# Performance work log

Hardware: AMD Instinct MI355X
Metric: run time of the kernel (lower is better)

Reference implementation:

```python
import jax, jax.numpy as jnp
import numpy as np

B, L = 8, 2048          # images, lines per image
C_IN, HW = 256, 128     # backbone feature channels, spatial size
DIM_LOI = 128
N_PTS0, N_PTS1 = 32, 8  # sampled points per line, after maxpool
SCALE = N_PTS0 // N_PTS1
EPS = 1e-5


def setup_inputs() -> dict:
    key = jax.random.key(0)
    ks = jax.random.split(key, 24)
    d = {}
    d['feature'] = jax.random.normal(ks[0], (B, C_IN, HW, HW), jnp.float32)
    # line endpoints in pixel coords [0, 128)
    d['lines'] = jax.random.uniform(ks[1], (B, L, 2, 2), jnp.float32) * HW
    # fc1: 1x1 conv 256 -> 128
    d['fc1_w'] = jax.random.normal(ks[2], (DIM_LOI, C_IN), jnp.float32) * 0.05
    d['fc1_b'] = jnp.zeros((DIM_LOI,), jnp.float32)
    planes = DIM_LOI // 2
    def bn(k, c):
        k1, k2, k3 = jax.random.split(k, 3)
        return (jax.random.normal(k1, (c,), jnp.float32) * 0.1 + 1.0,
                jax.random.normal(k2, (c,), jnp.float32) * 0.1,
                jax.random.normal(k3, (c,), jnp.float32) * 0.05,
                jax.random.uniform(jax.random.fold_in(k, 7), (c,), jnp.float32, 0.5, 1.5))
    d['bn1_g'], d['bn1_b'], d['bn1_m'], d['bn1_v'] = bn(ks[3], DIM_LOI)
    d['conv1_w'] = jax.random.normal(ks[4], (planes, DIM_LOI), jnp.float32) * 0.05
    d['conv1_b'] = jnp.zeros((planes,), jnp.float32)
    d['bn2_g'], d['bn2_b'], d['bn2_m'], d['bn2_v'] = bn(ks[5], planes)
    d['conv2_w'] = jax.random.normal(ks[6], (planes, planes, 3), jnp.float32) * 0.05
    d['conv2_b'] = jnp.zeros((planes,), jnp.float32)
    d['bn3_g'], d['bn3_b'], d['bn3_m'], d['bn3_v'] = bn(ks[7], planes)
    d['conv3_w'] = jax.random.normal(ks[8], (DIM_LOI, planes), jnp.float32) * 0.05
    d['conv3_b'] = jnp.zeros((DIM_LOI,), jnp.float32)
    d['fc2_w'] = jax.random.normal(ks[9], (1, DIM_LOI * N_PTS1), jnp.float32) * 0.02
    d['fc2_b'] = jnp.zeros((1,), jnp.float32)
    return d


def _bn(x, g, b, m, v):
    # x: [N, C, T], eval-mode batchnorm
    s = g * jax.lax.rsqrt(v + EPS)
    return x * s[None, :, None] + (b - m * s)[None, :, None]


def _loi_forward(feature, lines, fc1_w, fc1_b,
                 bn1_g, bn1_b, bn1_m, bn1_v, conv1_w, conv1_b,
                 bn2_g, bn2_b, bn2_m, bn2_v, conv2_w, conv2_b,
                 bn3_g, bn3_b, bn3_m, bn3_v, conv3_w, conv3_b,
                 fc2_w, fc2_b):
    # fc1: 1x1 conv -> [B, DIM_LOI, H, W]
    x = jnp.einsum('oc,bchw->bohw', fc1_w, feature) + fc1_b[None, :, None, None]

    # sample N_PTS0 points per line: p = p0*lam + p1*(1-lam) - 0.5
    lam = jnp.linspace(0.0, 1.0, N_PTS0, dtype=lines.dtype)  # [P]
    pts = (lines[:, :, 0, None, :] * lam[None, None, :, None]
           + lines[:, :, 1, None, :] * (1.0 - lam[None, None, :, None]) - 0.5)  # [B,L,P,2]
    px, py = pts[..., 0], pts[..., 1]
    px0 = jnp.clip(jnp.floor(px), 0.0, HW - 1.0)
    py0 = jnp.clip(jnp.floor(py), 0.0, HW - 1.0)
    px1 = jnp.clip(px0 + 1.0, 0.0, HW - 1.0)
    py1 = jnp.clip(py0 + 1.0, 0.0, HW - 1.0)
    px0l, py0l = px0.astype(jnp.int32), py0.astype(jnp.int32)
    px1l, py1l = px1.astype(jnp.int32), py1.astype(jnp.int32)

    def gather(f, ix, iy):  # f: [C,H,W], ix/iy: [L,P] -> [C,L,P]
        return f[:, ix, iy]

    gat = jax.vmap(gather)  # over batch
    xp = (gat(x, px0l, py0l) * ((px1 - px) * (py1 - py))[:, None]
          + gat(x, px1l, py0l) * ((px - px0) * (py1 - py))[:, None]
          + gat(x, px0l, py1l) * ((px1 - px) * (py - py0))[:, None]
          + gat(x, px1l, py1l) * ((px - px0) * (py - py0))[:, None])  # [B,C,L,P]

    xp = xp.transpose(0, 2, 1, 3).reshape(B * L, DIM_LOI, N_PTS0)  # [N,C,P]
    # MaxPool1d(kernel=stride=SCALE)
    xp = xp.reshape(B * L, DIM_LOI, N_PTS1, SCALE).max(axis=-1)  # [N,C,T=8]

    # Bottleneck1D residual: x + op(x)
    h = jax.nn.relu(_bn(xp, bn1_g, bn1_b, bn1_m, bn1_v))
    h = jnp.einsum('oc,nct->not', conv1_w, h) + conv1_b[None, :, None]
    h = jax.nn.relu(_bn(h, bn2_g, bn2_b, bn2_m, bn2_v))
    h = jax.lax.conv_general_dilated(h, conv2_w, (1,), [(1, 1)],
                                     dimension_numbers=('NCH', 'OIH', 'NCH'))
    h = h + conv2_b[None, :, None]
    h = jax.nn.relu(_bn(h, bn3_g, bn3_b, bn3_m, bn3_v))
    h = jnp.einsum('oc,nct->not', conv3_w, h) + conv3_b[None, :, None]
    xp = xp + h

    # fc2: ReLU -> Linear(dim_loi*n_pts1, 1)
    flat = jax.nn.relu(xp).reshape(B * L, DIM_LOI * N_PTS1)
    logits = (flat @ fc2_w.T + fc2_b).reshape(-1)  # [B*L]
    return logits


def reference(feature, lines, fc1_w, fc1_b,
              bn1_g, bn1_b, bn1_m, bn1_v, conv1_w, conv1_b,
              bn2_g, bn2_b, bn2_m, bn2_v, conv2_w, conv2_b,
              bn3_g, bn3_b, bn3_m, bn3_v, conv3_w, conv3_b,
              fc2_w, fc2_b):
    return _loi_forward(feature, lines, fc1_w, fc1_b,
                        bn1_g, bn1_b, bn1_m, bn1_v, conv1_w, conv1_b,
                        bn2_g, bn2_b, bn2_m, bn2_v, conv2_w, conv2_b,
                        bn3_g, bn3_b, bn3_m, bn3_v, conv3_w, conv3_b,
                        fc2_w, fc2_b)
```

## Files before the change

kernel.cpp:

```cpp
#include <hip/hip_runtime.h>

#define EPSBN 1e-5f

typedef _Float16 f16;
typedef _Float16 f16x8 __attribute__((ext_vector_type(8)));
typedef _Float16 f16x4 __attribute__((ext_vector_type(4)));
typedef _Float16 f16x2 __attribute__((ext_vector_type(2)));
typedef float    f32x4 __attribute__((ext_vector_type(4)));

__device__ inline unsigned int pack2(float a, float b) {
    union { f16x2 h; unsigned int u; } cv;
    cv.h[0] = (f16)a; cv.h[1] = (f16)b;
    return cv.u;
}
__device__ inline f16x4 hmax4(f16x4 a, f16x4 b) {
    f16x4 r;
    #pragma unroll
    for (int i = 0; i < 4; ++i) r[i] = a[i] > b[i] ? a[i] : b[i];
    return r;
}
__device__ inline f16x8 relu8(f16x8 v) {
    f16x8 r;
    #pragma unroll
    for (int i = 0; i < 8; ++i) r[i] = v[i] > (f16)0.f ? v[i] : (f16)0.f;
    return r;
}

__global__ void wprep_kernel(const float* __restrict__ fc1w,
                             const float* __restrict__ w1,
                             const float* __restrict__ w2,
                             const float* __restrict__ w3,
                             f16* __restrict__ dst) {
    const int i = blockIdx.x * 256 + threadIdx.x;
    float v;
    if (i < 32768)      v = fc1w[i];
    else if (i < 40960) v = w1[i - 32768];
    else if (i < 53248) {
        const int j = i - 40960, tau = j >> 12, rest = j & 4095;
        v = w2[rest * 3 + tau];
    } else              v = w3[i - 53248];
    dst[i] = (f16)v;
}

__global__ __launch_bounds__(256)
void fc1_mfma(const float* __restrict__ feat,
              const f16*   __restrict__ w16,
              const float* __restrict__ bias,
              f16*         __restrict__ xmap) {
    __shared__ f16 lds[64][136];

    const int tid  = threadIdx.x;
    const int wv   = tid >> 6, lane = tid & 63;
    const int n16  = lane & 15, quad = lane >> 4;
    const int b    = blockIdx.x & 7;
    const int p0   = (blockIdx.x >> 3) * 64;
    const int cp   = tid & 31;
    const int pg   = tid >> 5;

    f32x4 acc[8];
    #pragma unroll
    for (int nt = 0; nt < 8; ++nt) acc[nt] = (f32x4){0.f, 0.f, 0.f, 0.f};

    const float* fbase = feat + (((size_t)b) << 22) + p0 + pg * 8;
    unsigned int* ldsu = (unsigned int*)&lds[0][0];
    const int wrow = pg * 8;

    float4 c0a, c0b, c1a, c1b;
    {
        const float* r0 = fbase + (size_t)(2 * cp) * 16384;
        c0a = *(const float4*)(r0);          c0b = *(const float4*)(r0 + 4);
        c1a = *(const float4*)(r0 + 16384);  c1b = *(const float4*)(r0 + 16388);
        ldsu[(wrow + 0) * 68 + cp] = pack2(c0a.x, c1a.x);
        ldsu[(wrow + 1) * 68 + cp] = pack2(c0a.y, c1a.y);
        ldsu[(wrow + 2) * 68 + cp] = pack2(c0a.z, c1a.z);
        ldsu[(wrow + 3) * 68 + cp] = pack2(c0a.w, c1a.w);
        ldsu[(wrow + 4) * 68 + cp] = pack2(c0b.x, c1b.x);
        ldsu[(wrow + 5) * 68 + cp] = pack2(c0b.y, c1b.y);
        ldsu[(wrow + 6) * 68 + cp] = pack2(c0b.z, c1b.z);
        ldsu[(wrow + 7) * 68 + cp] = pack2(c0b.w, c1b.w);
    }

    for (int kc = 0; kc < 4; ++kc) {
        __syncthreads();
        if (kc < 3) {
            const float* r0 = fbase + (size_t)((kc + 1) * 64 + 2 * cp) * 16384;
            c0a = *(const float4*)(r0);          c0b = *(const float4*)(r0 + 4);
            c1a = *(const float4*)(r0 + 16384);  c1b = *(const float4*)(r0 + 16388);
        }
        #pragma unroll
        for (int ks = 0; ks < 2; ++ks) {
            const f16x8 a = *(const f16x8*)&lds[wv * 16 + n16][ks * 32 + quad * 8];
            #pragma unroll
            for (int nt = 0; nt < 8; ++nt) {
                const f16x8 bf = *(const f16x8*)&w16[(size_t)(nt * 16 + n16) * 256
                                                     + kc * 64 + ks * 32 + quad * 8];
                acc[nt] = __builtin_amdgcn_mfma_f32_16x16x32_f16(a, bf, acc[nt], 0, 0, 0);
            }
        }
        __syncthreads();
        if (kc < 3) {
            ldsu[(wrow + 0) * 68 + cp] = pack2(c0a.x, c1a.x);
            ldsu[(wrow + 1) * 68 + cp] = pack2(c0a.y, c1a.y);
            ldsu[(wrow + 2) * 68 + cp] = pack2(c0a.z, c1a.z);
            ldsu[(wrow + 3) * 68 + cp] = pack2(c0a.w, c1a.w);
            ldsu[(wrow + 4) * 68 + cp] = pack2(c0b.x, c1b.x);
            ldsu[(wrow + 5) * 68 + cp] = pack2(c0b.y, c1b.y);
            ldsu[(wrow + 6) * 68 + cp] = pack2(c0b.z, c1b.z);
            ldsu[(wrow + 7) * 68 + cp] = pack2(c0b.w, c1b.w);
        }
    }

    #pragma unroll
    for (int nt = 0; nt < 8; ++nt) {
        const int o = nt * 16 + n16;
        const float bo = bias[o];
        #pragma unroll
        for (int r = 0; r < 4; ++r)
            lds[wv * 16 + quad * 4 + r][o] = (f16)(acc[nt][r] + bo);
    }
    __syncthreads();

    #pragma unroll
    for (int it = 0; it < 4; ++it) {
        const int u = tid + 256 * it;
        const int row = u >> 4, cg = u & 15;
        const float4 v = *(const float4*)&lds[row][cg * 8];
        *(float4*)&xmap[(((size_t)((b << 14) + p0 + row)) << 7) + cg * 8] = v;
    }
}

__global__ __launch_bounds__(256)
void loi_kernel(const f16*   __restrict__ x,
                const float* __restrict__ lines,
                const f16*   __restrict__ wsp,
                const float* __restrict__ bn1g, const float* __restrict__ bn1b,
                const float* __restrict__ bn1m, const float* __restrict__ bn1v,
                const float* __restrict__ b1,
                const float* __restrict__ bn2g, const float* __restrict__ bn2b,
                const float* __restrict__ bn2m, const float* __restrict__ bn2v,
                const float* __restrict__ b2,
                const float* __restrict__ bn3g, const float* __restrict__ bn3b,
                const float* __restrict__ bn3m, const float* __restrict__ bn3v,
                const float* __restrict__ b3,
                const float* __restrict__ fc2w, const float* __restrict__ fc2b,
                float* __restrict__ out) {
    __shared__ f16 xp[64][136];
    __shared__ alignas(16) union {
        struct { int toff[256][4]; f16 twgt[256][4]; } tp;
        struct { f16 h1[80][72]; f16 h2[64][72]; } cv;
    } u;
    __shared__ f16 s1h[128], t1h[128];
    __shared__ float s2f[64], t2f[64], s3f[64], t3f[64], b1f[64], b2f[64];
    __shared__ float b3f[128];
    __shared__ float wsum[4][8];

    const f16* w1f16 = wsp + 32768;
    const f16* w2f16 = wsp + 40960;
    const f16* w3f16 = wsp + 53248;

    const int tid  = threadIdx.x;
    const int wv   = tid >> 6, lane = tid & 63;
    const int n16  = lane & 15, quad = lane >> 4;
    const int img  = blockIdx.x & 7;
    const int mblk = blockIdx.x >> 3;

    if (tid < 128) {
        const float s = bn1g[tid] * rsqrtf(bn1v[tid] + EPSBN);
        s1h[tid] = (f16)s; t1h[tid] = (f16)(bn1b[tid] - bn1m[tid] * s);
    }
    if (tid < 64) {
        const float s = bn2g[tid] * rsqrtf(bn2v[tid] + EPSBN);
        s2f[tid] = s; t2f[tid] = bn2b[tid] - bn2m[tid] * s;
        b1f[tid] = b1[tid];
    } else if (tid < 128) {
        const int c = tid - 64;
        const float s = bn3g[c] * rsqrtf(bn3v[c] + EPSBN);
        s3f[c] = s; t3f[c] = bn3b[c] - bn3m[c] * s;
        b2f[c] = b2[c];
    } else {
        b3f[tid - 128] = b3[tid - 128];
    }

    {
        const int li = tid >> 5, pt = tid & 31;
        const int gl = img * 2048 + mblk * 8 + li;
        const float4 ln = *(const float4*)&lines[gl * 4];
        const float lam = (float)pt * (1.0f / 31.0f);
        const float px = ln.x * lam + ln.z * (1.f - lam) - 0.5f;
        const float py = ln.y * lam + ln.w * (1.f - lam) - 0.5f;
        const float px0 = fminf(fmaxf(floorf(px), 0.f), 127.f);
        const float py0 = fminf(fmaxf(floorf(py), 0.f), 127.f);
        const float px1 = fminf(px0 + 1.f, 127.f);
        const float py1 = fminf(py0 + 1.f, 127.f);
        const int ix0 = (int)px0, iy0 = (int)py0;
        const int ix1 = (int)px1, iy1 = (int)py1;
        u.tp.toff[tid][0] = (((ix0 << 7) + iy0) << 7);
        u.tp.toff[tid][1] = (((ix1 << 7) + iy0) << 7);
        u.tp.toff[tid][2] = (((ix0 << 7) + iy1) << 7);
        u.tp.toff[tid][3] = (((ix1 << 7) + iy1) << 7);
        const float wx1 = px1 - px, wx0 = px - px0;
        const float wy1 = py1 - py, wy0 = py - py0;
        u.tp.twgt[tid][0] = (f16)(wx1 * wy1); u.tp.twgt[tid][1] = (f16)(wx0 * wy1);
        u.tp.twgt[tid][2] = (f16)(wx1 * wy0); u.tp.twgt[tid][3] = (f16)(wx0 * wy0);
    }
    __syncthreads();

    {
        const int h = lane >> 5, j = lane & 31;
        const int li = wv * 2 + h;
        const f16* xbh = x + (((size_t)img) << 21) + 4 * j;
        #pragma unroll
        for (int t = 0; t < 8; ++t) {
            f16x4 m = {(f16)(-60000.f), (f16)(-60000.f), (f16)(-60000.f), (f16)(-60000.f)};
            #pragma unroll
            for (int s = 0; s < 4; ++s) {
                const int combo = li * 32 + t * 4 + s;
                const int4  off = *(const int4*)&u.tp.toff[combo][0];
                const f16x4 tw  = *(const f16x4*)&u.tp.twgt[combo][0];
                const f16x4 g00 = *(const f16x4*)(xbh + off.x);
                const f16x4 g10 = *(const f16x4*)(xbh + off.y);
                const f16x4 g01 = *(const f16x4*)(xbh + off.z);
                const f16x4 g11 = *(const f16x4*)(xbh + off.w);
                const f16x4 w0 = {tw[0], tw[0], tw[0], tw[0]};
                const f16x4 w1v = {tw[1], tw[1], tw[1], tw[1]};
                const f16x4 w2v = {tw[2], tw[2], tw[2], tw[2]};
                const f16x4 w3v = {tw[3], tw[3], tw[3], tw[3]};
                f16x4 v = g00 * w0 + g10 * w1v + g01 * w2v + g11 * w3v;
                m = hmax4(m, v);
            }
            *(f16x4*)&xp[li * 8 + t][4 * j] = m;
        }
    }
    __syncthreads();

    {
        const int r = tid >> 4, seg = tid & 15;
        const int row = (r >> 1) * 10 + (r & 1) * 9;
        *(unsigned long long*)&u.cv.h1[row][seg * 4] = 0ull;
    }

    {
        const int o_lane = wv * 16 + n16;
        f32x4 acc1[4];
        #pragma unroll
        for (int nt = 0; nt < 4; ++nt) acc1[nt] = (f32x4){0.f, 0.f, 0.f, 0.f};
        #pragma unroll
        for (int ks = 0; ks < 4; ++ks) {
            const int k = ks * 32 + quad * 8;
            const f16x8 a  = *(const f16x8*)&w1f16[o_lane * 128 + k];
            const f16x8 s8 = *(const f16x8*)&s1h[k];
            const f16x8 t8 = *(const f16x8*)&t1h[k];
            #pragma unroll
            for (int nt = 0; nt < 4; ++nt) {
                const f16x8 raw = *(const f16x8*)&xp[nt * 16 + n16][k];
                const f16x8 bf = relu8(raw * s8 + t8);
                acc1[nt] = __builtin_amdgcn_mfma_f32_16x16x32_f16(a, bf, acc1[nt], 0, 0, 0);
            }
        }
        #pragma unroll
        for (int nt = 0; nt < 4; ++nt) {
            const int n = nt * 16 + n16;
            const int nprow = (n >> 3) * 10 + (n & 7) + 1;
            #pragma unroll
            for (int r = 0; r < 4; ++r) {
                const int o = wv * 16 + quad * 4 + r;
                const float v = fmaxf((acc1[nt][r] + b1f[o]) * s2f[o] + t2f[o], 0.f);
                u.cv.h1[nprow][o] = (f16)v;
            }
        }
    }
    __syncthreads();

    {
        const int o_lane = wv * 16 + n16;
        f32x4 acc2[4];
        #pragma unroll
        for (int nt = 0; nt < 4; ++nt) acc2[nt] = (f32x4){0.f, 0.f, 0.f, 0.f};
        #pragma unroll
        for (int d = 0; d < 3; ++d) {
            const f16* A2 = w2f16 + d * 4096;
            #pragma unroll
            for (int ks = 0; ks < 2; ++ks) {
                const int k = ks * 32 + quad * 8;
                const f16x8 a = *(const f16x8*)&A2[o_lane * 64 + k];
                #pragma unroll
                for (int nt = 0; nt < 4; ++nt) {
                    const int n = nt * 16 + n16;
                    const int row = (n >> 3) * 10 + (n & 7) + d;
                    const f16x8 bf = *(const f16x8*)&u.cv.h1[row][k];
                    acc2[nt] = __builtin_amdgcn_mfma_f32_16x16x32_f16(a, bf, acc2[nt], 0, 0, 0);
                }
            }
        }
        #pragma unroll
        for (int nt = 0; nt < 4; ++nt) {
            const int n = nt * 16 + n16;
            #pragma unroll
            for (int r = 0; r < 4; ++r) {
                const int o = wv * 16 + quad * 4 + r;
                const float v = fmaxf((acc2[nt][r] + b2f[o]) * s3f[o] + t3f[o], 0.f);
                u.cv.h2[n][o] = (f16)v;
            }
        }
    }
    __syncthreads();

    {
        const int col = n16 & 7, obase = wv * 16 + quad * 4;
        float fcv[2][4];
        #pragma unroll
        for (int h = 0; h < 2; ++h)
            #pragma unroll
            for (int r = 0; r < 4; ++r)
                fcv[h][r] = fc2w[(h * 64 + obase + r) * 8 + col];

        f32x4 acc3[2][4];
        #pragma unroll
        for (int h = 0; h < 2; ++h)
            #pragma unroll
            for (int nt = 0; nt < 4; ++nt) acc3[h][nt] = (f32x4){0.f, 0.f, 0.f, 0.f};
        #pragma unroll
        for (int ks = 0; ks < 2; ++ks) {
            const int k = ks * 32 + quad * 8;
            const f16x8 a0 = *(const f16x8*)&w3f16[(wv * 16 + n16) * 64 + k];
            const f16x8 a1 = *(const f16x8*)&w3f16[(64 + wv * 16 + n16) * 64 + k];
            #pragma unroll
            for (int nt = 0; nt < 4; ++nt) {
                const f16x8 bf = *(const f16x8*)&u.cv.h2[nt * 16 + n16][k];
                acc3[0][nt] = __builtin_amdgcn_mfma_f32_16x16x32_f16(a0, bf, acc3[0][nt], 0, 0, 0);
                acc3[1][nt] = __builtin_amdgcn_mfma_f32_16x16x32_f16(a1, bf, acc3[1][nt], 0, 0, 0);
            }
        }
        float part[4] = {0.f, 0.f, 0.f, 0.f};
        #pragma unroll
        for (int h = 0; h < 2; ++h) {
            const float4 bq = *(const float4*)&b3f[h * 64 + obase];
            const float bqa[4] = {bq.x, bq.y, bq.z, bq.w};
            #pragma unroll
            for (int nt = 0; nt < 4; ++nt) {
                const int n = nt * 16 + n16;
                const f16x4 rx = *(const f16x4*)&xp[n][h * 64 + obase];
                float p = 0.f;
                #pragma unroll
                for (int r = 0; r < 4; ++r) {
                    float v = acc3[h][nt][r] + bqa[r] + (float)rx[r];
                    v = fmaxf(v, 0.f);
                    p += v * fcv[h][r];
                }
                part[nt] += p;
            }
        }
        #pragma unroll
        for (int off_i = 0; off_i < 5; ++off_i) {
            const int off = (int[]){1, 2, 4, 16, 32}[off_i];
            part[0] += __shfl_xor(part[0], off, 64);
            part[1] += __shfl_xor(part[1], off, 64);
            part[2] += __shfl_xor(part[2], off, 64);
            part[3] += __shfl_xor(part[3], off, 64);
        }
        if ((lane & 55) == 0) {
            const int par = (lane >> 3) & 1;
            wsum[wv][0 + par] = part[0];
            wsum[wv][2 + par] = part[1];
            wsum[wv][4 + par] = part[2];
            wsum[wv][6 + par] = part[3];
        }
    }
    __syncthreads();

    if (tid < 8) {
        const float s = wsum[0][tid] + wsum[1][tid] + wsum[2][tid] + wsum[3][tid];
        out[img * 2048 + mblk * 8 + tid] = s + fc2b[0];
    }
}

extern "C" void kernel_launch(void* const* d_in, const int* in_sizes, int n_in,
                              void* d_out, int out_size, void* d_ws, size_t ws_size,
                              hipStream_t stream) {
    const float* feature = (const float*)d_in[0];
    const float* lines   = (const float*)d_in[1];
    const float* fc1_w   = (const float*)d_in[2];
    const float* fc1_b   = (const float*)d_in[3];
    const float* bn1g    = (const float*)d_in[4];
    const float* bn1b    = (const float*)d_in[5];
    const float* bn1m    = (const float*)d_in[6];
    const float* bn1v    = (const float*)d_in[7];
    const float* w1      = (const float*)d_in[8];
    const float* b1      = (const float*)d_in[9];
    const float* bn2g    = (const float*)d_in[10];
    const float* bn2b    = (const float*)d_in[11];
    const float* bn2m    = (const float*)d_in[12];
    const float* bn2v    = (const float*)d_in[13];
    const float* w2      = (const float*)d_in[14];
    const float* b2      = (const float*)d_in[15];
    const float* bn3g    = (const float*)d_in[16];
    const float* bn3b    = (const float*)d_in[17];
    const float* bn3m    = (const float*)d_in[18];
    const float* bn3v    = (const float*)d_in[19];
    const float* w3      = (const float*)d_in[20];
    const float* b3      = (const float*)d_in[21];
    const float* fc2w    = (const float*)d_in[22];
    const float* fc2b    = (const float*)d_in[23];

    f16* xmap = (f16*)d_ws;
    f16* wsp  = (f16*)((char*)d_ws + (size_t)32 * 1024 * 1024);

    wprep_kernel<<<240, 256, 0, stream>>>(fc1_w, w1, w2, w3, wsp);
    fc1_mfma<<<2048, 256, 0, stream>>>(feature, wsp, fc1_b, xmap);
    loi_kernel<<<2048, 256, 0, stream>>>(xmap, lines, wsp,
                                         bn1g, bn1b, bn1m, bn1v, b1,
                                         bn2g, bn2b, bn2m, bn2v, b2,
                                         bn3g, bn3b, bn3m, bn3v, b3,
                                         fc2w, fc2b, (float*)d_out);
}
```

Measured before the change: 324.9 us.

## Restructure fc1 GEMM with direct global-to-LDS double-buffered loads and larger tiles

Rewrites the fc1 1x1-conv kernel to use 512-thread blocks covering 256 pixels each. Feature channels are streamed straight into a double-buffered fp32 LDS tile with global_load_lds, and the fp16 conversion happens when fragments are read from LDS. This replaces the register staging and pack-and-store path and overlaps the next chunk's load with the current MFMAs. Weight fragments are reused across two pixel tiles. In exchange it uses more LDS per block, adds a strided fp32 LDS gather for the operand, and launches a quarter as many blocks.

```diff
diff --git a/kernel.cpp b/kernel.cpp
--- a/kernel.cpp
+++ b/kernel.cpp
@@ -42,90 +42,93 @@
     dst[i] = (f16)v;
 }
 
-__global__ __launch_bounds__(256)
+__global__ __launch_bounds__(512, 4)
 void fc1_mfma(const float* __restrict__ feat,
               const f16*   __restrict__ w16,
               const float* __restrict__ bias,
               f16*         __restrict__ xmap) {
-    __shared__ f16 lds[64][136];
+    __shared__ union {
+        float fbuf[2][8368];
+        f16   epi[256][136];
+    } u;
 
     const int tid  = threadIdx.x;
     const int wv   = tid >> 6, lane = tid & 63;
     const int n16  = lane & 15, quad = lane >> 4;
-    const int b    = blockIdx.x & 7;
-    const int p0   = (blockIdx.x >> 3) * 64;
-    const int cp   = tid & 31;
-    const int pg   = tid >> 5;
-
-    f32x4 acc[8];
+    const int img  = blockIdx.x & 7;
+    const int p0   = (blockIdx.x >> 3) << 8;
+
+    const float* fimg = feat + (((size_t)img) << 22);
+
+    f32x4 acc[8][2];
     #pragma unroll
-    for (int nt = 0; nt < 8; ++nt) acc[nt] = (f32x4){0.f, 0.f, 0.f, 0.f};
-
-    const float* fbase = feat + (((size_t)b) << 22) + p0 + pg * 8;
-    unsigned int* ldsu = (unsigned int*)&lds[0][0];
-    const int wrow = pg * 8;
-
-    float4 c0a, c0b, c1a, c1b;
-    {
-        const float* r0 = fbase + (size_t)(2 * cp) * 16384;
-        c0a = *(const float4*)(r0);          c0b = *(const float4*)(r0 + 4);
-        c1a = *(const float4*)(r0 + 16384);  c1b = *(const float4*)(r0 + 16388);
-        ldsu[(wrow + 0) * 68 + cp] = pack2(c0a.x, c1a.x);
-        ldsu[(wrow + 1) * 68 + cp] = pack2(c0a.y, c1a.y);
-        ldsu[(wrow + 2) * 68 + cp] = pack2(c0a.z, c1a.z);
-        ldsu[(wrow + 3) * 68 + cp] = pack2(c0a.w, c1a.w);
-        ldsu[(wrow + 4) * 68 + cp] = pack2(c0b.x, c1b.x);
-        ldsu[(wrow + 5) * 68 + cp] = pack2(c0b.y, c1b.y);
-        ldsu[(wrow + 6) * 68 + cp] = pack2(c0b.z, c1b.z);
-        ldsu[(wrow + 7) * 68 + cp] = pack2(c0b.w, c1b.w);
-    }
-
-    for (int kc = 0; kc < 4; ++kc) {
+    for (int ot = 0; ot < 8; ++ot) {
+        acc[ot][0] = (f32x4){0.f, 0.f, 0.f, 0.f};
+        acc[ot][1] = (f32x4){0.f, 0.f, 0.f, 0.f};
+    }
+
+    auto issue = [&](int s, int b) {
+        #pragma unroll
+        for (int i = 0; i < 4; ++i) {
+            const int cl = wv * 4 + i;
+            const int ch = s * 32 + cl;
+            const float* src = fimg + (((size_t)ch) << 14) + p0 + lane * 4;
+            float* dst = &u.fbuf[b][cl * 260 + (cl >> 3) * 16];
+            __builtin_amdgcn_global_load_lds(
+                (const __attribute__((address_space(1))) void*)src,
+                (__attribute__((address_space(3))) void*)dst, 16, 0, 0);
+        }
+    };
+
+    issue(0, 0);
+    __syncthreads();
+
+    for (int s = 0; s < 8; ++s) {
+        const int cur = s & 1;
+        if (s < 7) issue(s + 1, cur ^ 1);
+
+        f16x8 xf[2];
+        #pragma unroll
+        for (int pt = 0; pt < 2; ++pt) {
+            const int pbase = wv * 32 + pt * 16 + n16;
+            const float* fb = &u.fbuf[cur][quad * 16 + pbase];
+            f16x8 xv;
+            #pragma unroll
+            for (int j = 0; j < 8; ++j)
+                xv[j] = (f16)fb[(quad * 8 + j) * 260];
+            xf[pt] = xv;
+        }
+
+        const f16* wrow = w16 + (size_t)n16 * 256 + s * 32 + quad * 8;
+        #pragma unroll
+        for (int ot = 0; ot < 8; ++ot) {
+            const f16x8 wf = *(const f16x8*)(wrow + ot * 4096);
+            acc[ot][0] = __builtin_amdgcn_mfma_f32_16x16x32_f16(wf, xf[0], acc[ot][0], 0, 0, 0);
+            acc[ot][1] = __builtin_amdgcn_mfma_f32_16x16x32_f16(wf, xf[1], acc[ot][1], 0, 0, 0);
+        }
         __syncthreads();
-        if (kc < 3) {
-            const float* r0 = fbase + (size_t)((kc + 1) * 64 + 2 * cp) * 16384;
-            c0a = *(const float4*)(r0);          c0b = *(const float4*)(r0 + 4);
-            c1a = *(const float4*)(r0 + 16384);  c1b = *(const float4*)(r0 + 16388);
-        }
-        #pragma unroll
-        for (int ks = 0; ks < 2; ++ks) {
-            const f16x8 a = *(const f16x8*)&lds[wv * 16 + n16][ks * 32 + quad * 8];
-            #pragma unroll
-            for (int nt = 0; nt < 8; ++nt) {
-                const f16x8 bf = *(const f16x8*)&w16[(size_t)(nt * 16 + n16) * 256
-                                                     + kc * 64 + ks * 32 + quad * 8];
-                acc[nt] = __builtin_amdgcn_mfma_f32_16x16x32_f16(a, bf, acc[nt], 0, 0, 0);
-            }
-        }
-        __syncthreads();
-        if (kc < 3) {
-            ldsu[(wrow + 0) * 68 + cp] = pack2(c0a.x, c1a.x);
-            ldsu[(wrow + 1) * 68 + cp] = pack2(c0a.y, c1a.y);
-            ldsu[(wrow + 2) * 68 + cp] = pack2(c0a.z, c1a.z);
-            ldsu[(wrow + 3) * 68 + cp] = pack2(c0a.w, c1a.w);
-            ldsu[(wrow + 4) * 68 + cp] = pack2(c0b.x, c1b.x);
-            ldsu[(wrow + 5) * 68 + cp] = pack2(c0b.y, c1b.y);
-            ldsu[(wrow + 6) * 68 + cp] = pack2(c0b.z, c1b.z);
-            ldsu[(wrow + 7) * 68 + cp] = pack2(c0b.w, c1b.w);
-        }
     }
 
     #pragma unroll
-    for (int nt = 0; nt < 8; ++nt) {
-        const int o = nt * 16 + n16;
-        const float bo = bias[o];
-        #pragma unroll
-        for (int r = 0; r < 4; ++r)
-            lds[wv * 16 + quad * 4 + r][o] = (f16)(acc[nt][r] + bo);
+    for (int ot = 0; ot < 8; ++ot) {
+        const float4 bq = *(const float4*)&bias[ot * 16 + quad * 4];
+        const float bqa[4] = {bq.x, bq.y, bq.z, bq.w};
+        #pragma unroll
+        for (int pt = 0; pt < 2; ++pt) {
+            f16x4 h;
+            #pragma unroll
+            for (int r = 0; r < 4; ++r) h[r] = (f16)(acc[ot][pt][r] + bqa[r]);
+            *(f16x4*)&u.epi[wv * 32 + pt * 16 + n16][ot * 16 + quad * 4] = h;
+        }
     }
     __syncthreads();
 
     #pragma unroll
-    for (int it = 0; it < 4; ++it) {
-        const int u = tid + 256 * it;
-        const int row = u >> 4, cg = u & 15;
-        const float4 v = *(const float4*)&lds[row][cg * 8];
-        *(float4*)&xmap[(((size_t)((b << 14) + p0 + row)) << 7) + cg * 8] = v;
+    for (int it = 0; it < 8; ++it) {
+        const int idx = it * 512 + tid;
+        const int row = idx >> 4, seg = idx & 15;
+        const float4 v = *(const float4*)&u.epi[row][seg * 8];
+        *(float4*)&xmap[(((size_t)(img * 16384 + p0 + row)) << 7) + seg * 8] = v;
     }
 }
 
@@ -406,7 +409,7 @@
     f16* wsp  = (f16*)((char*)d_ws + (size_t)32 * 1024 * 1024);
 
     wprep_kernel<<<240, 256, 0, stream>>>(fc1_w, w1, w2, w3, wsp);
-    fc1_mfma<<<2048, 256, 0, stream>>>(feature, wsp, fc1_b, xmap);
+    fc1_mfma<<<512, 512, 0, stream>>>(feature, wsp, fc1_b, xmap);
     loi_kernel<<<2048, 256, 0, stream>>>(xmap, lines, wsp,
                                          bn1g, bn1b, bn1m, bn1v, b1,
                                          bn2g, bn2b, bn2m, bn2v, b2,
```

After: 293.5 us. -9.7%, faster.
